# Performance work log

Hardware: AMD Instinct MI355X
Metric: run time of the kernel (lower is better)

Reference implementation:

```python
import jax, jax.numpy as jnp
import numpy as np
import math
from functools import lru_cache

# ---------- Clebsch-Gordan machinery (numpy, setup-time only) ----------

def _cg(j1, m1, j2, m2, j, m):
    """Complex-basis CG coefficient via Racah's formula (Condon-Shortley)."""
    if m1 + m2 != m:
        return 0.0
    f = math.factorial
    pre = (2 * j + 1) * f(j1 + j2 - j) * f(j1 - j2 + j) * f(-j1 + j2 + j) / f(j1 + j2 + j + 1)
    pre *= f(j1 + m1) * f(j1 - m1) * f(j2 + m2) * f(j2 - m2) * f(j + m) * f(j - m)
    s = 0.0
    for k in range(0, j1 + j2 - j + 1):
        d = (k, j1 + j2 - j - k, j1 - m1 - k, j2 + m2 - k, j - j2 + m1 + k, j - j1 - m2 + k)
        if min(d) < 0:
            continue
        s += (-1) ** k / (f(d[0]) * f(d[1]) * f(d[2]) * f(d[3]) * f(d[4]) * f(d[5]))
    return math.sqrt(pre) * s


def _csh_to_rsh(j):
    """Unitary complex->real spherical harmonics transform, columns indexed by real m."""
    C = np.zeros((2 * j + 1, 2 * j + 1), dtype=np.complex128)
    s2 = 1.0 / math.sqrt(2.0)
    for m in range(-j, j + 1):
        am = abs(m)
        if m < 0:
            C[j + m, j + m] = 1j * s2
            C[j - m, j + m] = -1j * ((-1) ** am) * s2
        elif m == 0:
            C[j, j] = 1.0
        else:
            C[j - m, j + m] = s2
            C[j + m, j + m] = ((-1) ** am) * s2
    return C


@lru_cache(maxsize=None)
def _rsh_cg(j1, j2, j):
    """Real-basis CG, compactified to rows [m1, m2, m, coeff] over nonzeros."""
    csh = np.zeros((2 * j1 + 1, 2 * j2 + 1, 2 * j + 1), dtype=np.complex128)
    for m1 in range(-j1, j1 + 1):
        for m2 in range(-j2, j2 + 1):
            m = m1 + m2
            if -j <= m <= j:
                csh[j1 + m1, j2 + m2, j + m] = _cg(j1, m1, j2, m2, j, m)
    r = np.einsum('abc,ai,bj,ck->ijk', csh, _csh_to_rsh(j1), _csh_to_rsh(j2), np.conj(_csh_to_rsh(j)))
    r = np.real(r * ((-1j) ** (j1 + j2 + j)))
    m1g, m2g, mg = np.meshgrid(np.arange(-j1, j1 + 1), np.arange(-j2, j2 + 1),
                               np.arange(-j, j + 1), indexing='ij')
    mask = np.abs(r) > 1e-12
    return np.stack([m1g[mask].astype(np.float64), m2g[mask].astype(np.float64),
                     mg[mask].astype(np.float64), r[mask]], axis=0)


def _build_coupler(md1, md2, trunc_in=True):
    """Faithful replay of CGPCoupler._init_params: returns cg_tilde, repids, out_dim."""
    md1 = np.asarray(md1, dtype=np.int64)
    md2 = np.asarray(md2, dtype=np.int64)
    md_in = np.stack([md1, md2], axis=0)                      # [2, 2*(L+1)]
    max_n_out = np.maximum(md1, md2)
    nlp = md_in.shape[1]
    n_irr = np.repeat(np.arange(nlp // 2) * 2 + 1, 2)         # irreps per (l,p) slot
    off_in = np.cumsum(md_in * n_irr[None, :], axis=1)
    off_in = np.concatenate([np.zeros((2, 1), dtype=np.int64), off_in[:, :-1]], axis=1)
    max_l = nlp // 2 - 1
    md_out = np.zeros_like(max_n_out)
    valid = []
    for lout in range(max_l + 1):
        for pout in (1, -1):
            for l1 in range(max_l + 1):
                for l2 in range(max_l + 1):
                    for p1 in (1, -1):
                        for p2 in (1, -1):
                            cp = (-1) ** (lout + l1 + l2)
                            if p1 * p2 * cp != pout:
                                continue
                            if l1 + l2 < lout or abs(l1 - l2) > lout:
                                continue
                            lp1 = 2 * l1 + (1 - p1) // 2
                            lp2 = 2 * l2 + (1 - p2) // 2
                            lpo = 2 * lout + (1 - pout) // 2
                            if trunc_in:
                                if l1 + l2 > max_l:
                                    continue
                                deg = min(md_in[0, lp1], md_in[1, lp2],
                                          max_n_out[2 * (l1 + l2) + (1 - pout) // 2])
                            else:
                                deg = min(md_in[0, lp1], md_in[1, lp2], max_n_out[lpo])
                            md_out[lpo] += deg
                            if deg > 0:
                                valid.append((lpo, lp1, lp2, int(deg)))
    off_out = np.cumsum(md_out * n_irr)
    off_out = np.concatenate([[0], off_out[:-1]]).astype(np.int64)
    cg_l, r1_l, r2_l, ro_l = [], [], [], []
    ns_off, lpo_last = 0, 0
    for lpo, lp1, lp2, deg in valid:
        if lpo > lpo_last:
            ns_off = 0
        l1, l2, lout = lp1 // 2, lp2 // 2, lpo // 2
        src = _rsh_cg(l1, l2, lout)                            # [4, nnz]
        seg = np.repeat(src, deg, axis=1)                      # repeat_interleave along dim=1
        ns = np.tile(np.arange(deg, dtype=np.int64), src.shape[1])
        r1_l.append(off_in[0, lp1] + np.rint(seg[0] + l1).astype(np.int64) * md_in[0, lp1] + ns)
        r2_l.append(off_in[1, lp2] + np.rint(seg[1] + l2).astype(np.int64) * md_in[1, lp2] + ns)
        ro_l.append(off_out[lpo] + np.rint(seg[2] + lout).astype(np.int64) * md_out[lpo] + ns_off + ns)
        cg_l.append(seg[3])
        ns_off += deg
        lpo_last = lpo
    out_dim = int(np.sum(md_out * n_irr))
    return (np.concatenate(cg_l), np.concatenate(r1_l), np.concatenate(r2_l),
            np.concatenate(ro_l), out_dim)


METADATA = [32, 32, 32, 32, 32, 32, 32, 32]   # max_l = 3, 32 channels per (l, parity)
BATCH = 2048


def setup_inputs() -> dict:
    key = jax.random.key(0)
    k1, k2 = jax.random.split(key)
    cg, r1, r2, ro, out_dim = _build_coupler(METADATA, METADATA, trunc_in=True)
    n_irr = np.repeat(np.arange(len(METADATA) // 2) * 2 + 1, 2)
    in_dim = int(np.sum(np.asarray(METADATA) * n_irr))        # 1024
    x1 = jax.random.normal(k1, (BATCH, in_dim), dtype=jnp.float32)
    x2 = jax.random.normal(k2, (BATCH, in_dim), dtype=jnp.float32)
    return {
        "x1": x1,
        "x2": x2,
        "cg_tilde": jnp.asarray(cg, dtype=jnp.float32),
        "repids_in1": jnp.asarray(r1, dtype=jnp.int64) if jax.config.jax_enable_x64 else jnp.asarray(r1, dtype=jnp.int32),
        "repids_in2": jnp.asarray(r2, dtype=jnp.int64) if jax.config.jax_enable_x64 else jnp.asarray(r2, dtype=jnp.int32),
        "repids_out": jnp.asarray(ro, dtype=jnp.int64) if jax.config.jax_enable_x64 else jnp.asarray(ro, dtype=jnp.int32),
        "out_dim": out_dim,
    }


def reference(x1, x2, cg_tilde, repids_in1, repids_in2, repids_out, out_dim):
    # gather along rep dim (last), elementwise multiply with CG coeffs, scatter-add
    out_tilde = x1[:, repids_in1] * x2[:, repids_in2] * cg_tilde[None, :]   # [B, K]
    out = jnp.zeros((x1.shape[0], out_dim), dtype=x1.dtype).at[:, repids_out].add(out_tilde)
    return out
```

## Files before the change

### kernel.cpp

```cpp
#include <hip/hip_runtime.h>


#define IN_DIM  1024
#define ROWS    8
#define NOBCAP  512
#define SKIP_OB 511u

typedef float f32x2 __attribute__((ext_vector_type(2)));
typedef float f32x4 __attribute__((ext_vector_type(4)));

__global__ __launch_bounds__(1024) void prep_kernel(
    const int* __restrict__ r1, const int* __restrict__ r2,
    const int* __restrict__ ro, const float* __restrict__ cg,
    int nseg, int nob,
    uint2* __restrict__ qdesc, uint2* __restrict__ ddesc,
    int* __restrict__ zlist, int* __restrict__ hdr)
{
    __shared__ int cntS[NOBCAP], rankS[NOBCAP];
    __shared__ int qoffS[NOBCAP], doffS[NOBCAP];
    __shared__ int wsum[8], woff[8];
    const int t = threadIdx.x;

    if (t < NOBCAP) { cntS[t] = 0; rankS[t] = 0; }
    __syncthreads();

    for (int s = t; s < nseg; s += 1024)
        atomicAdd(&cntS[ro[s << 5] >> 5], 1);
    __syncthreads();

    int c = 0;
    unsigned int pv = 0;
    if (t < NOBCAP) {
        c = (t < nob) ? cntS[t] : 0;
        const int q  = (t < nob && c >= 3) ? ((c + 3) >> 2) : 0;
        const int df = (t < nob && c <= 2) ? 1 : 0;
        const int zf = (t < nob && c > 4) ? 1 : 0;
        pv = ((unsigned int)q << 20) | ((unsigned int)df << 10) | (unsigned int)zf;
    }
    const int lane = t & 63;
    const int wid  = t >> 6;
    #pragma unroll
    for (int off = 1; off < 64; off <<= 1) {
        const unsigned int n = __shfl_up(pv, off, 64);
        if (lane >= off) pv += n;
    }
    if (t < NOBCAP && lane == 63) wsum[wid] = (int)pv;
    __syncthreads();
    if (t < 8) {
        unsigned int v = (unsigned int)wsum[t];
        const unsigned int self = v;
        #pragma unroll
        for (int off = 1; off < 8; off <<= 1) {
            const unsigned int n = __shfl_up(v, off, 64);
            if (t >= off) v += n;
        }
        woff[t] = (int)(v - self);
    }
    __syncthreads();

    if (t < NOBCAP) {
        const unsigned int incl = pv + (unsigned int)woff[wid];
        const int qi = (incl >> 20) & 1023;
        const int di = (incl >> 10) & 1023;
        const int zi = incl & 1023;
        if (t < nob) {
            if (c <= 2) {
                const int db = di - 1;
                doffS[t] = db;
                const unsigned int pd = ((unsigned int)t << 20) | 0x80000000u;
                for (int j = (db << 1) + c; j < ((db + 1) << 1); ++j)
                    ddesc[j] = make_uint2(pd, 0u);
            } else {
                const int qn = (c + 3) >> 2;
                const int qb = qi - qn;
                qoffS[t] = qb;
                const unsigned int fl = (c > 4) ? 0u : 0x80000000u;
                if (c > 4) zlist[zi - 1] = t;
                const unsigned int pd = ((unsigned int)t << 20) | fl;
                for (int j = (qb << 2) + c; j < ((qb + qn) << 2); ++j)
                    qdesc[j] = make_uint2(pd, 0u);
            }
        }
        if (t == NOBCAP - 1) {
            const int nq = qi, nd = di;
            const int nqPad = (nq + 15) & ~15;
            const int ndPad = (nd + 31) & ~31;
            const uint2 dummy = make_uint2(SKIP_OB << 20, 0u);
            for (int j = (nq << 2); j < (nqPad << 2); ++j) qdesc[j] = dummy;
            for (int j = (nd << 1); j < (ndPad << 1); ++j) ddesc[j] = dummy;
            hdr[0] = nqPad; hdr[1] = zi; hdr[2] = ndPad;
        }
    }
    __syncthreads();

    for (int s = t; s < nseg; s += 1024) {
        const int k  = s << 5;
        const int ob = ro[k] >> 5;
        const int cc = cntS[ob];
        const int rk = atomicAdd(&rankS[ob], 1);
        const unsigned int fl = (cc > 4) ? 0u : 0x80000000u;
        const uint2 v = make_uint2((unsigned int)r1[k] | ((unsigned int)r2[k] << 10)
                                   | ((unsigned int)ob << 20) | fl,
                                   __float_as_uint(cg[k]));
        if (cc <= 2) ddesc[(doffS[ob] << 1) + rk] = v;
        else         qdesc[(qoffS[ob] << 2) + rk] = v;
    }
}

__device__ __forceinline__ void accum4(f32x2& lo, f32x2& hi,
                                       unsigned int dx, unsigned int dc,
                                       const float* xs1, const float* xs2)
{
    const float  c = __uint_as_float(dc);
    const f32x4 u = *reinterpret_cast<const f32x4*>(xs1 + (dx & 1023u));
    const f32x4 v = *reinterpret_cast<const f32x4*>(xs2 + ((dx >> 10) & 1023u));
    const f32x2 cc  = {c, c};
    const f32x2 u01 = {u.x, u.y}, u23 = {u.z, u.w};
    const f32x2 v01 = {v.x, v.y}, v23 = {v.z, v.w};
    lo += cc * (u01 * v01);
    hi += cc * (u23 * v23);
}

__device__ __forceinline__ void terminal(float* orow, unsigned int hx,
                                         f32x2 lo, f32x2 hi)
{
    const int ob = (int)((hx >> 20) & 511u);
    if (ob == (int)SKIP_OB) return;
    float* p = orow + (ob << 5);
    if (hx >> 31) {
        const f32x4 st = {lo.x, lo.y, hi.x, hi.y};
        __builtin_nontemporal_store(st, reinterpret_cast<f32x4*>(p));
    } else {
        unsafeAtomicAdd(p,     lo.x);
        unsafeAtomicAdd(p + 1, lo.y);
        unsafeAtomicAdd(p + 2, hi.x);
        unsafeAtomicAdd(p + 3, hi.y);
    }
}

__global__ __launch_bounds__(1024) void cgp_main(const float* __restrict__ x1,
    const float* __restrict__ x2, const uint2* __restrict__ qdesc,
    const uint2* __restrict__ ddesc, const int* __restrict__ zlist,
    const int* __restrict__ hdr, float* __restrict__ out, int out_dim)
{
    __shared__ float x1s[ROWS * IN_DIM];
    __shared__ float x2s[ROWS * IN_DIM];
    const int r0  = blockIdx.x * ROWS;
    const int tid = threadIdx.x;

    {
        const f32x4* p1 = reinterpret_cast<const f32x4*>(x1 + (size_t)r0 * IN_DIM);
        const f32x4* p2 = reinterpret_cast<const f32x4*>(x2 + (size_t)r0 * IN_DIM);
        f32x4* s1 = reinterpret_cast<f32x4*>(x1s);
        f32x4* s2 = reinterpret_cast<f32x4*>(x2s);
        #pragma unroll
        for (int j = tid; j < (ROWS * IN_DIM) >> 2; j += 1024) {
            s1[j] = __builtin_nontemporal_load(p1 + j);
            s2[j] = __builtin_nontemporal_load(p2 + j);
        }
    }
    const int nz = hdr[1];
    for (int i = tid; i < (nz << 5); i += 1024) {
        const int ob = zlist[i >> 5];
        const int ch = i & 31;
        float* p = out + (size_t)r0 * out_dim + (ob << 5) + ch;
        #pragma unroll
        for (int j = 0; j < ROWS; ++j)
            __builtin_nontemporal_store(0.f, p + j * out_dim);
    }
    __syncthreads();

    const int w  = tid >> 6;
    const int ln = tid & 63;
    const int rr = ln >> 3;
    const int tt = ln & 7;
    const float* xs1 = x1s + rr * IN_DIM + (tt << 2);
    const float* xs2 = x2s + rr * IN_DIM + (tt << 2);
    float* orow = out + (size_t)(r0 + rr) * out_dim + (tt << 2);

    {
        const int qpw = hdr[0] >> 4;
        const uint2* qd = qdesc + ((size_t)(w * qpw) << 2);
        #pragma unroll 2
        for (int i = 0; i < qpw; ++i, qd += 4) {
            const uint4 A  = *reinterpret_cast<const uint4*>(qd);
            const uint4 Bq = *reinterpret_cast<const uint4*>(qd + 2);
            f32x2 lo = {0.f, 0.f}, hi = {0.f, 0.f};
            accum4(lo, hi, A.x,  A.y,  xs1, xs2);
            accum4(lo, hi, A.z,  A.w,  xs1, xs2);
            accum4(lo, hi, Bq.x, Bq.y, xs1, xs2);
            accum4(lo, hi, Bq.z, Bq.w, xs1, xs2);
            terminal(orow, A.x, lo, hi);
        }
    }

    {
        const int ppw = hdr[2] >> 5;
        const uint2* dd = ddesc + ((size_t)(w * ppw) << 2);
        #pragma unroll 2
        for (int i = 0; i < ppw; ++i, dd += 4) {
            const uint4 A  = *reinterpret_cast<const uint4*>(dd);
            const uint4 Bq = *reinterpret_cast<const uint4*>(dd + 2);
            f32x2 l0 = {0.f, 0.f}, h0 = {0.f, 0.f};
            f32x2 l1 = {0.f, 0.f}, h1 = {0.f, 0.f};
            accum4(l0, h0, A.x,  A.y,  xs1, xs2);
            accum4(l0, h0, A.z,  A.w,  xs1, xs2);
            accum4(l1, h1, Bq.x, Bq.y, xs1, xs2);
            accum4(l1, h1, Bq.z, Bq.w, xs1, xs2);
            terminal(orow, A.x,  l0, h0);
            terminal(orow, Bq.x, l1, h1);
        }
    }
}

extern "C" void kernel_launch(void* const* d_in, const int* in_sizes, int n_in,
                              void* d_out, int out_size, void* d_ws, size_t ws_size,
                              hipStream_t stream)
{
    const float* x1 = (const float*)d_in[0];
    const float* x2 = (const float*)d_in[1];
    const float* cg = (const float*)d_in[2];
    const int*   r1 = (const int*)d_in[3];
    const int*   r2 = (const int*)d_in[4];
    const int*   ro = (const int*)d_in[5];
    float* out = (float*)d_out;

    const int B       = in_sizes[0] / IN_DIM;
    const int out_dim = out_size / B;
    const int K       = in_sizes[2];
    const int nseg    = K >> 5;
    const int nob     = out_dim >> 5;
    const int qcap    = nob + (nseg >> 2) + 32;
    const int dcap    = nob + 48;

    auto align16 = [](size_t v) { return (v + 15) & ~(size_t)15; };
    char* ws = (char*)d_ws;
    uint2* qdesc = (uint2*)ws;  ws += align16((size_t)qcap * 4 * sizeof(uint2));
    uint2* ddesc = (uint2*)ws;  ws += align16((size_t)dcap * 2 * sizeof(uint2));
    int*   zlist = (int*)ws;    ws += align16((size_t)NOBCAP * sizeof(int));
    int*   hdr   = (int*)ws;

    hipLaunchKernelGGL(prep_kernel, dim3(1), dim3(1024), 0, stream,
                       r1, r2, ro, cg, nseg, nob, qdesc, ddesc, zlist, hdr);
    hipLaunchKernelGGL(cgp_main, dim3(B / ROWS), dim3(1024), 0, stream,
                       x1, x2, qdesc, ddesc, zlist, hdr, out, out_dim);
}
```

Baseline: 26.54 us.

## Fuse descriptor prep into main kernel, building descriptors per block in LDS

Removes the separate single-block prep kernel. Each block now rebuilds the segment descriptors, zero list and header in shared memory, then runs the gather-multiply-scatter. The x1/x2 tile loads are issued into registers before the prep work so their latency overlaps the LDS scan. This drops a kernel launch and the serial dependency on one 1024-thread block, at the cost of every block repeating the prep and using fixed LDS capacities (QSLOTS/DSLOTS, zlist of 128) that must fit the problem.

```diff
diff --git a/kernel.cpp b/kernel.cpp
--- a/kernel.cpp
+++ b/kernel.cpp
@@ -5,31 +5,89 @@
 #define ROWS    8
 #define NOBCAP  512
 #define SKIP_OB 511u
+#define QSLOTS  1024
+#define DSLOTS  640
 
 typedef float f32x2 __attribute__((ext_vector_type(2)));
 typedef float f32x4 __attribute__((ext_vector_type(4)));
 
-__global__ __launch_bounds__(1024) void prep_kernel(
+#define BAR_LDS() do { asm volatile("s_waitcnt lgkmcnt(0)" ::: "memory"); \
+                       __builtin_amdgcn_s_barrier(); } while (0)
+#define BAR_ALL() do { asm volatile("s_waitcnt vmcnt(0) lgkmcnt(0)" ::: "memory"); \
+                       __builtin_amdgcn_s_barrier(); } while (0)
+
+__device__ __forceinline__ void accum4(f32x2& lo, f32x2& hi,
+                                       unsigned int dx, unsigned int dc,
+                                       const float* xs1, const float* xs2)
+{
+    const float c = __uint_as_float(dc);
+    const f32x4 u = *reinterpret_cast<const f32x4*>(xs1 + (dx & 1023u));
+    const f32x4 v = *reinterpret_cast<const f32x4*>(xs2 + ((dx >> 10) & 1023u));
+    const f32x2 cc  = {c, c};
+    const f32x2 u01 = {u.x, u.y}, u23 = {u.z, u.w};
+    const f32x2 v01 = {v.x, v.y}, v23 = {v.z, v.w};
+    lo += cc * (u01 * v01);
+    hi += cc * (u23 * v23);
+}
+
+__device__ __forceinline__ void terminal(float* orow, unsigned int hx,
+                                         f32x2 lo, f32x2 hi)
+{
+    const int ob = (int)((hx >> 20) & 511u);
+    if (ob == (int)SKIP_OB) return;
+    float* p = orow + (ob << 5);
+    if (hx >> 31) {
+        const f32x4 st = {lo.x, lo.y, hi.x, hi.y};
+        __builtin_nontemporal_store(st, reinterpret_cast<f32x4*>(p));
+    } else {
+        unsafeAtomicAdd(p,     lo.x);
+        unsafeAtomicAdd(p + 1, lo.y);
+        unsafeAtomicAdd(p + 2, hi.x);
+        unsafeAtomicAdd(p + 3, hi.y);
+    }
+}
+
+__global__ __launch_bounds__(1024) void cgp_fused(
+    const float* __restrict__ x1, const float* __restrict__ x2,
     const int* __restrict__ r1, const int* __restrict__ r2,
     const int* __restrict__ ro, const float* __restrict__ cg,
-    int nseg, int nob,
-    uint2* __restrict__ qdesc, uint2* __restrict__ ddesc,
-    int* __restrict__ zlist, int* __restrict__ hdr)
-{
+    int nseg, int nob, float* __restrict__ out, int out_dim)
+{
+    __shared__ __align__(16) float x1s[ROWS * IN_DIM];
+    __shared__ __align__(16) float x2s[ROWS * IN_DIM];
+    __shared__ __align__(16) uint2 qdescL[QSLOTS];
+    __shared__ __align__(16) uint2 ddescL[DSLOTS];
     __shared__ int cntS[NOBCAP], rankS[NOBCAP];
     __shared__ int qoffS[NOBCAP], doffS[NOBCAP];
     __shared__ int wsum[8], woff[8];
-    const int t = threadIdx.x;
+    __shared__ int zlistL[128];
+    __shared__ int hdrL[4];
+
+    const int t  = threadIdx.x;
+    const int r0 = blockIdx.x * ROWS;
 
     if (t < NOBCAP) { cntS[t] = 0; rankS[t] = 0; }
-    __syncthreads();
+
+    int roV = 0, r1V = 0, r2V = 0; float cgV = 0.f;
+    if (t < nseg) {
+        const int k = t << 5;
+        roV = ro[k]; r1V = r1[k]; r2V = r2[k]; cgV = cg[k];
+    }
+
+    const f32x4* p1 = reinterpret_cast<const f32x4*>(x1 + (size_t)r0 * IN_DIM);
+    const f32x4* p2 = reinterpret_cast<const f32x4*>(x2 + (size_t)r0 * IN_DIM);
+    const f32x4 sA = __builtin_nontemporal_load(p1 + t);
+    const f32x4 sB = __builtin_nontemporal_load(p1 + t + 1024);
+    const f32x4 sC = __builtin_nontemporal_load(p2 + t);
+    const f32x4 sD = __builtin_nontemporal_load(p2 + t + 1024);
+
+    BAR_LDS();
 
     for (int s = t; s < nseg; s += 1024)
-        atomicAdd(&cntS[ro[s << 5] >> 5], 1);
-    __syncthreads();
-
-    int c = 0;
-    unsigned int pv = 0;
+        atomicAdd(&cntS[((s == t) ? roV : ro[s << 5]) >> 5], 1);
+    BAR_LDS();
+
+    int c = 0; unsigned int pv = 0;
     if (t < NOBCAP) {
         c = (t < nob) ? cntS[t] : 0;
         const int q  = (t < nob && c >= 3) ? ((c + 3) >> 2) : 0;
@@ -37,15 +95,14 @@
         const int zf = (t < nob && c > 4) ? 1 : 0;
         pv = ((unsigned int)q << 20) | ((unsigned int)df << 10) | (unsigned int)zf;
     }
-    const int lane = t & 63;
-    const int wid  = t >> 6;
+    const int lane = t & 63, wid = t >> 6;
     #pragma unroll
     for (int off = 1; off < 64; off <<= 1) {
         const unsigned int n = __shfl_up(pv, off, 64);
         if (lane >= off) pv += n;
     }
     if (t < NOBCAP && lane == 63) wsum[wid] = (int)pv;
-    __syncthreads();
+    BAR_LDS();
     if (t < 8) {
         unsigned int v = (unsigned int)wsum[t];
         const unsigned int self = v;
@@ -56,7 +113,7 @@
         }
         woff[t] = (int)(v - self);
     }
-    __syncthreads();
+    BAR_LDS();
 
     if (t < NOBCAP) {
         const unsigned int incl = pv + (unsigned int)woff[wid];
@@ -69,16 +126,16 @@
                 doffS[t] = db;
                 const unsigned int pd = ((unsigned int)t << 20) | 0x80000000u;
                 for (int j = (db << 1) + c; j < ((db + 1) << 1); ++j)
-                    ddesc[j] = make_uint2(pd, 0u);
+                    ddescL[j] = make_uint2(pd, 0u);
             } else {
                 const int qn = (c + 3) >> 2;
                 const int qb = qi - qn;
                 qoffS[t] = qb;
                 const unsigned int fl = (c > 4) ? 0u : 0x80000000u;
-                if (c > 4) zlist[zi - 1] = t;
+                if (c > 4) zlistL[zi - 1] = t;
                 const unsigned int pd = ((unsigned int)t << 20) | fl;
                 for (int j = (qb << 2) + c; j < ((qb + qn) << 2); ++j)
-                    qdesc[j] = make_uint2(pd, 0u);
+                    qdescL[j] = make_uint2(pd, 0u);
             }
         }
         if (t == NOBCAP - 1) {
@@ -86,92 +143,46 @@
             const int nqPad = (nq + 15) & ~15;
             const int ndPad = (nd + 31) & ~31;
             const uint2 dummy = make_uint2(SKIP_OB << 20, 0u);
-            for (int j = (nq << 2); j < (nqPad << 2); ++j) qdesc[j] = dummy;
-            for (int j = (nd << 1); j < (ndPad << 1); ++j) ddesc[j] = dummy;
-            hdr[0] = nqPad; hdr[1] = zi; hdr[2] = ndPad;
-        }
-    }
-    __syncthreads();
+            for (int j = (nq << 2); j < (nqPad << 2); ++j) qdescL[j] = dummy;
+            for (int j = (nd << 1); j < (ndPad << 1); ++j) ddescL[j] = dummy;
+            hdrL[0] = nqPad; hdrL[1] = zi; hdrL[2] = ndPad;
+        }
+    }
+    BAR_LDS();
 
     for (int s = t; s < nseg; s += 1024) {
-        const int k  = s << 5;
-        const int ob = ro[k] >> 5;
+        int ob, rv1, rv2; float cgx;
+        if (s == t) { ob = roV >> 5; rv1 = r1V; rv2 = r2V; cgx = cgV; }
+        else { const int k = s << 5; ob = ro[k] >> 5; rv1 = r1[k]; rv2 = r2[k]; cgx = cg[k]; }
         const int cc = cntS[ob];
         const int rk = atomicAdd(&rankS[ob], 1);
         const unsigned int fl = (cc > 4) ? 0u : 0x80000000u;
-        const uint2 v = make_uint2((unsigned int)r1[k] | ((unsigned int)r2[k] << 10)
+        const uint2 v = make_uint2((unsigned int)rv1 | ((unsigned int)rv2 << 10)
                                    | ((unsigned int)ob << 20) | fl,
-                                   __float_as_uint(cg[k]));
-        if (cc <= 2) ddesc[(doffS[ob] << 1) + rk] = v;
-        else         qdesc[(qoffS[ob] << 2) + rk] = v;
-    }
-}
-
-__device__ __forceinline__ void accum4(f32x2& lo, f32x2& hi,
-                                       unsigned int dx, unsigned int dc,
-                                       const float* xs1, const float* xs2)
-{
-    const float  c = __uint_as_float(dc);
-    const f32x4 u = *reinterpret_cast<const f32x4*>(xs1 + (dx & 1023u));
-    const f32x4 v = *reinterpret_cast<const f32x4*>(xs2 + ((dx >> 10) & 1023u));
-    const f32x2 cc  = {c, c};
-    const f32x2 u01 = {u.x, u.y}, u23 = {u.z, u.w};
-    const f32x2 v01 = {v.x, v.y}, v23 = {v.z, v.w};
-    lo += cc * (u01 * v01);
-    hi += cc * (u23 * v23);
-}
-
-__device__ __forceinline__ void terminal(float* orow, unsigned int hx,
-                                         f32x2 lo, f32x2 hi)
-{
-    const int ob = (int)((hx >> 20) & 511u);
-    if (ob == (int)SKIP_OB) return;
-    float* p = orow + (ob << 5);
-    if (hx >> 31) {
-        const f32x4 st = {lo.x, lo.y, hi.x, hi.y};
-        __builtin_nontemporal_store(st, reinterpret_cast<f32x4*>(p));
-    } else {
-        unsafeAtomicAdd(p,     lo.x);
-        unsafeAtomicAdd(p + 1, lo.y);
-        unsafeAtomicAdd(p + 2, hi.x);
-        unsafeAtomicAdd(p + 3, hi.y);
-    }
-}
-
-__global__ __launch_bounds__(1024) void cgp_main(const float* __restrict__ x1,
-    const float* __restrict__ x2, const uint2* __restrict__ qdesc,
-    const uint2* __restrict__ ddesc, const int* __restrict__ zlist,
-    const int* __restrict__ hdr, float* __restrict__ out, int out_dim)
-{
-    __shared__ float x1s[ROWS * IN_DIM];
-    __shared__ float x2s[ROWS * IN_DIM];
-    const int r0  = blockIdx.x * ROWS;
-    const int tid = threadIdx.x;
+                                   __float_as_uint(cgx));
+        if (cc <= 2) ddescL[(doffS[ob] << 1) + rk] = v;
+        else         qdescL[(qoffS[ob] << 2) + rk] = v;
+    }
 
     {
-        const f32x4* p1 = reinterpret_cast<const f32x4*>(x1 + (size_t)r0 * IN_DIM);
-        const f32x4* p2 = reinterpret_cast<const f32x4*>(x2 + (size_t)r0 * IN_DIM);
         f32x4* s1 = reinterpret_cast<f32x4*>(x1s);
         f32x4* s2 = reinterpret_cast<f32x4*>(x2s);
-        #pragma unroll
-        for (int j = tid; j < (ROWS * IN_DIM) >> 2; j += 1024) {
-            s1[j] = __builtin_nontemporal_load(p1 + j);
-            s2[j] = __builtin_nontemporal_load(p2 + j);
-        }
-    }
-    const int nz = hdr[1];
-    for (int i = tid; i < (nz << 5); i += 1024) {
-        const int ob = zlist[i >> 5];
-        const int ch = i & 31;
+        s1[t] = sA; s1[t + 1024] = sB;
+        s2[t] = sC; s2[t + 1024] = sD;
+    }
+
+    const int nz = hdrL[1];
+    for (int i = t; i < (nz << 5); i += 1024) {
+        const int ob = zlistL[i >> 5], ch = i & 31;
         float* p = out + (size_t)r0 * out_dim + (ob << 5) + ch;
         #pragma unroll
         for (int j = 0; j < ROWS; ++j)
             __builtin_nontemporal_store(0.f, p + j * out_dim);
     }
-    __syncthreads();
-
-    const int w  = tid >> 6;
-    const int ln = tid & 63;
+    BAR_ALL();
+
+    const int w  = t >> 6;
+    const int ln = t & 63;
     const int rr = ln >> 3;
     const int tt = ln & 7;
     const float* xs1 = x1s + rr * IN_DIM + (tt << 2);
@@ -179,8 +190,8 @@
     float* orow = out + (size_t)(r0 + rr) * out_dim + (tt << 2);
 
     {
-        const int qpw = hdr[0] >> 4;
-        const uint2* qd = qdesc + ((size_t)(w * qpw) << 2);
+        const int qpw = hdrL[0] >> 4;
+        const uint2* qd = qdescL + ((size_t)(w * qpw) << 2);
         #pragma unroll 2
         for (int i = 0; i < qpw; ++i, qd += 4) {
             const uint4 A  = *reinterpret_cast<const uint4*>(qd);
@@ -193,10 +204,9 @@
             terminal(orow, A.x, lo, hi);
         }
     }
-
     {
-        const int ppw = hdr[2] >> 5;
-        const uint2* dd = ddesc + ((size_t)(w * ppw) << 2);
+        const int ppw = hdrL[2] >> 5;
+        const uint2* dd = ddescL + ((size_t)(w * ppw) << 2);
         #pragma unroll 2
         for (int i = 0; i < ppw; ++i, dd += 4) {
             const uint4 A  = *reinterpret_cast<const uint4*>(dd);
@@ -230,18 +240,7 @@
     const int K       = in_sizes[2];
     const int nseg    = K >> 5;
     const int nob     = out_dim >> 5;
-    const int qcap    = nob + (nseg >> 2) + 32;
-    const int dcap    = nob + 48;
-
-    auto align16 = [](size_t v) { return (v + 15) & ~(size_t)15; };
-    char* ws = (char*)d_ws;
-    uint2* qdesc = (uint2*)ws;  ws += align16((size_t)qcap * 4 * sizeof(uint2));
-    uint2* ddesc = (uint2*)ws;  ws += align16((size_t)dcap * 2 * sizeof(uint2));
-    int*   zlist = (int*)ws;    ws += align16((size_t)NOBCAP * sizeof(int));
-    int*   hdr   = (int*)ws;
-
-    hipLaunchKernelGGL(prep_kernel, dim3(1), dim3(1024), 0, stream,
-                       r1, r2, ro, cg, nseg, nob, qdesc, ddesc, zlist, hdr);
-    hipLaunchKernelGGL(cgp_main, dim3(B / ROWS), dim3(1024), 0, stream,
-                       x1, x2, qdesc, ddesc, zlist, hdr, out, out_dim);
-}
+
+    hipLaunchKernelGGL(cgp_fused, dim3(B / ROWS), dim3(1024), 0, stream,
+                       x1, x2, r1, r2, ro, cg, nseg, nob, out, out_dim);
+}
```

Result: no change. 26.27 us (median of 2 runs) (-1.0%).

## Halve rows per block and split each wave into two half-waves over descriptors

Applied to the files above, without the earlier changes.

Each block now handles 4 rows instead of 8, which doubles the grid size and halves the shared memory per block. To keep all 64 lanes busy, each wave is split into two 32-lane halves that process alternate descriptor groups, and the descriptor padding is raised to match. The aim is more blocks per CU and better occupancy and latency hiding. In exchange, every descriptor is loaded by both halves, and the per-row overhead of loading descriptors roughly doubles across the grid.

```diff
diff --git a/kernel.cpp b/kernel.cpp
--- a/kernel.cpp
+++ b/kernel.cpp
@@ -2,7 +2,7 @@
 
 
 #define IN_DIM  1024
-#define ROWS    8
+#define ROWS    4
 #define NOBCAP  512
 #define SKIP_OB 511u
 
@@ -83,8 +83,8 @@
         }
         if (t == NOBCAP - 1) {
             const int nq = qi, nd = di;
-            const int nqPad = (nq + 15) & ~15;
-            const int ndPad = (nd + 31) & ~31;
+            const int nqPad = (nq + 31) & ~31;
+            const int ndPad = (nd + 63) & ~63;
             const uint2 dummy = make_uint2(SKIP_OB << 20, 0u);
             for (int j = (nq << 2); j < (nqPad << 2); ++j) qdesc[j] = dummy;
             for (int j = (nd << 1); j < (ndPad << 1); ++j) ddesc[j] = dummy;
@@ -111,7 +111,7 @@
                                        unsigned int dx, unsigned int dc,
                                        const float* xs1, const float* xs2)
 {
-    const float  c = __uint_as_float(dc);
+    const float c = __uint_as_float(dc);
     const f32x4 u = *reinterpret_cast<const f32x4*>(xs1 + (dx & 1023u));
     const f32x4 v = *reinterpret_cast<const f32x4*>(xs2 + ((dx >> 10) & 1023u));
     const f32x2 cc  = {c, c};
@@ -138,7 +138,7 @@
     }
 }
 
-__global__ __launch_bounds__(1024) void cgp_main(const float* __restrict__ x1,
+__global__ __launch_bounds__(1024, 8) void cgp_main(const float* __restrict__ x1,
     const float* __restrict__ x2, const uint2* __restrict__ qdesc,
     const uint2* __restrict__ ddesc, const int* __restrict__ zlist,
     const int* __restrict__ hdr, float* __restrict__ out, int out_dim)
@@ -153,10 +153,9 @@
         const f32x4* p2 = reinterpret_cast<const f32x4*>(x2 + (size_t)r0 * IN_DIM);
         f32x4* s1 = reinterpret_cast<f32x4*>(x1s);
         f32x4* s2 = reinterpret_cast<f32x4*>(x2s);
-        #pragma unroll
-        for (int j = tid; j < (ROWS * IN_DIM) >> 2; j += 1024) {
-            s1[j] = __builtin_nontemporal_load(p1 + j);
-            s2[j] = __builtin_nontemporal_load(p2 + j);
+        if (tid < (ROWS * IN_DIM) >> 2) {
+            s1[tid] = __builtin_nontemporal_load(p1 + tid);
+            s2[tid] = __builtin_nontemporal_load(p2 + tid);
         }
     }
     const int nz = hdr[1];
@@ -172,8 +171,10 @@
 
     const int w  = tid >> 6;
     const int ln = tid & 63;
-    const int rr = ln >> 3;
-    const int tt = ln & 7;
+    const bool hi = (ln >> 5) != 0;
+    const int hl = ln & 31;
+    const int rr = hl >> 3;
+    const int tt = hl & 7;
     const float* xs1 = x1s + rr * IN_DIM + (tt << 2);
     const float* xs2 = x2s + rr * IN_DIM + (tt << 2);
     float* orow = out + (size_t)(r0 + rr) * out_dim + (tt << 2);
@@ -181,26 +182,32 @@
     {
         const int qpw = hdr[0] >> 4;
         const uint2* qd = qdesc + ((size_t)(w * qpw) << 2);
-        #pragma unroll 2
-        for (int i = 0; i < qpw; ++i, qd += 4) {
-            const uint4 A  = *reinterpret_cast<const uint4*>(qd);
-            const uint4 Bq = *reinterpret_cast<const uint4*>(qd + 2);
-            f32x2 lo = {0.f, 0.f}, hi = {0.f, 0.f};
-            accum4(lo, hi, A.x,  A.y,  xs1, xs2);
-            accum4(lo, hi, A.z,  A.w,  xs1, xs2);
-            accum4(lo, hi, Bq.x, Bq.y, xs1, xs2);
-            accum4(lo, hi, Bq.z, Bq.w, xs1, xs2);
-            terminal(orow, A.x, lo, hi);
+        for (int i = 0; i < qpw; i += 2, qd += 8) {
+            const uint4 A0 = *reinterpret_cast<const uint4*>(qd);
+            const uint4 B0 = *reinterpret_cast<const uint4*>(qd + 2);
+            const uint4 A1 = *reinterpret_cast<const uint4*>(qd + 4);
+            const uint4 B1 = *reinterpret_cast<const uint4*>(qd + 6);
+            const uint4 A  = hi ? A1 : A0;
+            const uint4 Bq = hi ? B1 : B0;
+            f32x2 lo = {0.f, 0.f}, hh = {0.f, 0.f};
+            accum4(lo, hh, A.x,  A.y,  xs1, xs2);
+            accum4(lo, hh, A.z,  A.w,  xs1, xs2);
+            accum4(lo, hh, Bq.x, Bq.y, xs1, xs2);
+            accum4(lo, hh, Bq.z, Bq.w, xs1, xs2);
+            terminal(orow, A.x, lo, hh);
         }
     }
 
     {
-        const int ppw = hdr[2] >> 5;
-        const uint2* dd = ddesc + ((size_t)(w * ppw) << 2);
-        #pragma unroll 2
-        for (int i = 0; i < ppw; ++i, dd += 4) {
-            const uint4 A  = *reinterpret_cast<const uint4*>(dd);
-            const uint4 Bq = *reinterpret_cast<const uint4*>(dd + 2);
+        const int dpw = hdr[2] >> 4;
+        const uint2* dd = ddesc + ((size_t)(w * dpw) << 1);
+        for (int i = 0; i < dpw; i += 4, dd += 8) {
+            const uint4 A0 = *reinterpret_cast<const uint4*>(dd);
+            const uint4 B0 = *reinterpret_cast<const uint4*>(dd + 2);
+            const uint4 A1 = *reinterpret_cast<const uint4*>(dd + 4);
+            const uint4 B1 = *reinterpret_cast<const uint4*>(dd + 6);
+            const uint4 A  = hi ? A1 : A0;
+            const uint4 Bq = hi ? B1 : B0;
             f32x2 l0 = {0.f, 0.f}, h0 = {0.f, 0.f};
             f32x2 l1 = {0.f, 0.f}, h1 = {0.f, 0.f};
             accum4(l0, h0, A.x,  A.y,  xs1, xs2);
@@ -230,8 +237,8 @@
     const int K       = in_sizes[2];
     const int nseg    = K >> 5;
     const int nob     = out_dim >> 5;
-    const int qcap    = nob + (nseg >> 2) + 32;
-    const int dcap    = nob + 48;
+    const int qcap    = nob + (nseg >> 2) + 64;
+    const int dcap    = nob + 96;
 
     auto align16 = [](size_t v) { return (v + 15) & ~(size_t)15; };
     char* ws = (char*)d_ws;
```

After: 28.31 us. 1.07x slower.
